# Kernel tuning notes

Measured on AMD Instinct MI355X. Metric: run time of the kernel, lower is better.

The kernel has to match this reference:

```python
import jax, jax.numpy as jnp
import numpy as np

_SAMPLING_EPS = 1e-5
NEG_INF = jnp.float32(-jnp.inf)


def setup_inputs() -> dict:
    key = jax.random.key(0)
    k1, k2, k3, k4, k5 = jax.random.split(key, 5)
    B, V = 128, 128000
    logits = jax.random.normal(k1, (B, V), dtype=jnp.float32) * 4.0
    # every 8th row is greedy (temperature 0), rest random in [0.1, 1.5)
    rand_t = 0.1 + 1.4 * jax.random.uniform(k2, (B,), dtype=jnp.float32)
    temperatures = jnp.where(jnp.arange(B) % 8 == 0, 0.0, rand_t)
    top_k = jax.random.randint(k3, (B,), 1, 1001, dtype=jnp.int64)
    top_p = 0.1 + 0.9 * jax.random.uniform(k4, (B,), dtype=jnp.float32)
    # q ~ Exponential(1), replaces torch's generator-based q.exponential_()
    exp_noise = jax.random.exponential(k5, (B, V), dtype=jnp.float32)
    return {"logits": logits, "temperatures": temperatures, "top_k": top_k,
            "top_p": top_p, "exp_noise": exp_noise}


def _masked_logits(logits, temperatures, top_k, top_p):
    B, V = logits.shape
    # apply_temperature: greedy rows (temp < eps) divide by 1.0
    temp = jnp.where(temperatures < _SAMPLING_EPS, 1.0, temperatures)
    x = logits / temp[:, None]                       # [B, V]
    # ascending sort (as in torch code)
    sort_idx = jnp.argsort(x, axis=-1)               # [B, V]
    x_sort = jnp.take_along_axis(x, sort_idx, axis=-1)
    # top-k: keep the k largest (last k of ascending sort)
    k = jnp.clip(top_k, None, V).astype(jnp.int32)
    thr_idx = (V - k)[:, None]                       # [B, 1]
    thr = jnp.take_along_axis(x_sort, thr_idx, axis=-1)
    x_sort = jnp.where(x_sort < thr, NEG_INF, x_sort)
    # top-p on the sorted (ascending) logits
    probs_sort = jax.nn.softmax(x_sort, axis=-1)
    probs_sum = jnp.cumsum(probs_sort, axis=-1)
    p_mask = probs_sum <= (1.0 - top_p)[:, None]
    p_mask = p_mask.at[:, -1].set(False)             # always keep the max
    x_sort = jnp.where(p_mask, NEG_INF, x_sort)
    # scatter back to original positions: out[b, sort_idx[b, j]] = x_sort[b, j]
    rows = jnp.arange(B)[:, None]
    return x.at[rows, sort_idx].set(x_sort)


def reference(logits, temperatures, top_k, top_p, exp_noise):
    logits = logits.astype(jnp.float32)
    greedy = jnp.argmax(logits, axis=-1)             # [B]
    masked = _masked_logits(logits, temperatures, top_k, top_p)
    probs = jax.nn.softmax(masked, axis=-1)
    # Gumbel-max / exponential-race sampling: argmax(probs / q)
    random_sampled = jnp.argmax(probs / exp_noise, axis=-1)
    sampled = jnp.where(temperatures < _SAMPLING_EPS, greedy, random_sampled)
    return sampled[:, None].astype(jnp.int32)        # SamplerOutput.sampled_token_ids
```

## Files before the change

kernel.cpp:

```cpp
#include <hip/hip_runtime.h>
#include <stdint.h>

#define CAP 4096
#define SL 20
#define THR1 256
#define THR4 1024
#define SEPS 1e-5f
#define ZMAX 8
#define LBUF 1024
#define KTHRF 8.0f
#define NB 4096
#define NBSH 13

typedef unsigned long long ull;

__device__ __forceinline__ uint32_t f2key(float x) {
  uint32_t u = __float_as_uint(x);
  return u ^ ((u & 0x80000000u) ? 0xFFFFFFFFu : 0x80000000u);
}
__device__ __forceinline__ float key2f(uint32_t k) {
  uint32_t u = (k & 0x80000000u) ? (k ^ 0x80000000u) : ~k;
  return __uint_as_float(u);
}

__global__ void k1_cap(const float* __restrict__ logits, const float* __restrict__ noise,
                       const float* __restrict__ temps,
                       ull* __restrict__ cand, unsigned int* __restrict__ cnt,
                       ull* __restrict__ rowmax, unsigned int* __restrict__ zcnt,
                       int* __restrict__ zlist, int B, int V, int slice_len) {
  __shared__ ull s_buf[LBUF];
  __shared__ unsigned int s_n, s_base;
  __shared__ ull s_w64[THR1 / 64];
  int tid = threadIdx.x;
  int lane = tid & 63, wid = tid >> 6;
  int half = B * SL;
  int bid = blockIdx.x;
  bool noise_side = bid >= half;
  if (noise_side) bid -= half;
  int row = bid / SL;
  int slice = bid % SL;
  float tr = temps[row];
  int col_base = slice * slice_len;
  int n4 = slice_len >> 2;
  int pairs = n4 >> 1;

  if (noise_side) {
    if (tr < SEPS) return;
    const float4* q4 = reinterpret_cast<const float4*>(noise + (size_t)row * V + col_base);
    for (int p = tid; p < pairs; p += THR1) {
      int v = p << 1;
      float4 q0 = q4[v];
      float4 q1 = q4[v + 1];
      float qs[8] = {q0.x, q0.y, q0.z, q0.w, q1.x, q1.y, q1.z, q1.w};
      bool anyz = (qs[0] == 0.f) | (qs[1] == 0.f) | (qs[2] == 0.f) | (qs[3] == 0.f) |
                  (qs[4] == 0.f) | (qs[5] == 0.f) | (qs[6] == 0.f) | (qs[7] == 0.f);
      if (anyz) {
        int c0 = col_base + 8 * p;
#pragma unroll
        for (int m = 0; m < 8; ++m) {
          if (qs[m] == 0.0f) {
            unsigned int zp = atomicAdd(&zcnt[row], 1u);
            if (zp < ZMAX) zlist[row * ZMAX + zp] = c0 + m;
          }
        }
      }
    }
    return;
  }

  const float4* p4 = reinterpret_cast<const float4*>(logits + (size_t)row * V + col_base);
  if (tr < SEPS) {
    ull best = 0ULL;
    for (int p = tid; p < pairs; p += THR1) {
      int v = p << 1;
      float4 f0 = p4[v];
      float4 f1 = p4[v + 1];
      int c0 = col_base + 8 * p;
      float xs[8] = {f0.x, f0.y, f0.z, f0.w, f1.x, f1.y, f1.z, f1.w};
#pragma unroll
      for (int m = 0; m < 8; ++m) {
        ull pk = ((ull)f2key(xs[m]) << 32) | (ull)(uint32_t)(V - 1 - (c0 + m));
        if (pk > best) best = pk;
      }
    }
    for (int off = 32; off > 0; off >>= 1) {
      ull o = __shfl_down(best, off);
      if (o > best) best = o;
    }
    if (lane == 0) s_w64[wid] = best;
    __syncthreads();
    if (tid == 0) {
      ull b2 = s_w64[0];
      for (int w = 1; w < THR1 / 64; ++w) if (s_w64[w] > b2) b2 = s_w64[w];
      atomicMax(&rowmax[row], b2);
    }
    return;
  }

  if (tid == 0) s_n = 0;
  __syncthreads();
  for (int p0 = 0; p0 < pairs; p0 += THR1) {
    int p = p0 + tid;
    unsigned int cm = 0;
    float fs[8];
    if (p < pairs) {
      int v = p << 1;
      float4 f0 = p4[v];
      float4 f1 = p4[v + 1];
      fs[0] = f0.x; fs[1] = f0.y; fs[2] = f0.z; fs[3] = f0.w;
      fs[4] = f1.x; fs[5] = f1.y; fs[6] = f1.z; fs[7] = f1.w;
#pragma unroll
      for (int m = 0; m < 8; ++m) cm |= (fs[m] >= KTHRF) ? (1u << m) : 0u;
    }
    unsigned int c8 = (unsigned int)__popc(cm);
    unsigned int inc = c8;
    for (int off = 1; off < 64; off <<= 1) {
      unsigned int o = __shfl_up(inc, off);
      if (lane >= off) inc += o;
    }
    unsigned int total = __shfl(inc, 63);
    if (total) {
      unsigned int base = 0;
      if (lane == 0) base = atomicAdd(&s_n, total);
      base = __shfl(base, 0);
      unsigned int off0 = base + inc - c8;
      if (cm) {
        int c0 = col_base + 8 * p;
#pragma unroll
        for (int m = 0; m < 8; ++m) {
          if (cm & (1u << m)) {
            uint32_t key = __float_as_uint(fs[m]) ^ 0x80000000u;
            ull pk = ((ull)key << 32) | (ull)(uint32_t)(c0 + m);
            if (off0 < LBUF) s_buf[off0] = pk;
            else {
              unsigned int g = atomicAdd(&cnt[row], 1u);
              if (g < CAP) cand[(size_t)row * CAP + g] = pk;
            }
            off0++;
          }
        }
      }
    }
  }
  __syncthreads();
  unsigned int m = (s_n < LBUF) ? s_n : LBUF;
  if (tid == 0) s_base = atomicAdd(&cnt[row], m);
  __syncthreads();
  unsigned int base = s_base;
  for (unsigned int i = tid; i < m; i += THR1) {
    unsigned int g = base + i;
    if (g < CAP) cand[(size_t)row * CAP + g] = s_buf[i];
  }
}

__global__ __launch_bounds__(THR4) void k4_final(
    const ull* __restrict__ cand, const unsigned int* __restrict__ cnt,
    const int* __restrict__ topk32, const float* __restrict__ temps,
    const float* __restrict__ topp, const float* __restrict__ noise,
    const ull* __restrict__ rowmax, const unsigned int* __restrict__ zcnt,
    const int* __restrict__ zlist, int* __restrict__ out, int B, int V) {
  __shared__ ull s_cand[CAP];
  __shared__ float s_e[CAP];
  __shared__ float s_q[CAP];
  __shared__ unsigned char s_kept[CAP];
  __shared__ float s_w[16];
  __shared__ unsigned int s_u[16];
  __shared__ ull s_w64[16];
  __shared__ int s_nan, s_pz, s_flag, s_pbin, s_m;
  int tid = threadIdx.x, row = blockIdx.x;
  int lane = tid & 63, wid = tid >> 6;
  float tr = temps[row];
  if (tr < SEPS) {
    if (tid == 0) {
      ull rm = rowmax[row];
      out[row] = V - 1 - (int)(uint32_t)(rm & 0xFFFFFFFFu);
    }
    return;
  }
  if (tid == 0) { s_nan = 0x7FFFFFFF; s_flag = 0; }
  unsigned int* hist = (unsigned int*)s_e;
  for (int b = tid; b < NB; b += THR4) hist[b] = 0;
  __syncthreads();
  if (tid < B && topk32[tid] == 0) s_flag = 1;

  unsigned int cv = cnt[row];
  int n = (cv < (unsigned int)CAP) ? (int)cv : CAP;
  if (n < 1) n = 1;
  uint32_t Kb = f2key(KTHRF / tr);
  ull held[4]; int nh = 0;
  for (int i = tid; i < n; i += THR4) {
    ull c = cand[(size_t)row * CAP + i];
    float x = key2f((uint32_t)(c >> 32)) / tr;
    uint32_t xk = f2key(x);
    held[nh++] = ((ull)xk << 32) | (c & 0xFFFFFFFFu);
    uint32_t bin = (xk - Kb) >> NBSH;
    if (bin > NB - 1) bin = NB - 1;
    atomicAdd(&hist[bin], 1u);
  }
  __syncthreads();
  int kraw = s_flag ? topk32[2 * row] : topk32[row];
  int kk = kraw < 1 ? 1 : (kraw > V ? V : kraw);
  if (kk > n) kk = n;
  unsigned int hb[4], csum = 0;
#pragma unroll
  for (int c = 0; c < 4; ++c) { hb[c] = hist[(tid << 2) + c]; csum += hb[c]; }
  unsigned int sfx = csum;
  for (int off = 1; off < 64; off <<= 1) {
    unsigned int o = __shfl_down(sfx, off);
    if (lane + off < 64) sfx += o;
  }
  if (lane == 0) s_u[wid] = sfx;
  __syncthreads();
  unsigned int above = sfx - csum;
  for (int w = wid + 1; w < 16; ++w) above += s_u[w];
  unsigned int run0 = above;
  for (int c = 3; c >= 0; --c) {
    unsigned int prev = run0;
    run0 += hb[c];
    if (run0 >= (unsigned int)kk && prev < (unsigned int)kk) {
      s_pbin = (tid << 2) + c;
      s_m = (int)run0;
    }
  }
  __syncthreads();
  uint32_t Pk = Kb + ((uint32_t)s_pbin << NBSH);
  int m = s_m;
  int myc = 0;
#pragma unroll
  for (int j = 0; j < 4; ++j)
    if (j < nh && (uint32_t)(held[j] >> 32) >= Pk) myc++;
  unsigned int inc = (unsigned int)myc;
  for (int off = 1; off < 64; off <<= 1) {
    unsigned int o = __shfl_up(inc, off);
    if (lane >= off) inc += o;
  }
  if (lane == 63) s_u[wid] = inc;
  __syncthreads();
  unsigned int base = inc - (unsigned int)myc;
  for (int w = 0; w < wid; ++w) base += s_u[w];
  int wpos = 0;
#pragma unroll
  for (int j = 0; j < 4; ++j)
    if (j < nh && (uint32_t)(held[j] >> 32) >= Pk) s_cand[base + (wpos++)] = held[j];
  int N = 64;
  while (N < m) N <<= 1;
  __syncthreads();
  for (int i = m + tid; i < N; i += THR4) s_cand[i] = 0ULL;
  __syncthreads();
  for (int k = 2; k <= 64; k <<= 1) {
    for (int j = k >> 1; j > 0; j >>= 1) {
      for (int i = tid; i < N; i += THR4) {
        int l = i ^ j;
        if (l > i) {
          ull a = s_cand[i], b = s_cand[l];
          bool up = ((i & k) == 0);
          if (up ? (a < b) : (a > b)) { s_cand[i] = b; s_cand[l] = a; }
        }
      }
      __builtin_amdgcn_wave_barrier();
    }
  }
  __syncthreads();
  for (int k = 128; k <= N; k <<= 1) {
    for (int j = k >> 1; j >= 64; j >>= 1) {
      for (int i = tid; i < N; i += THR4) {
        int l = i ^ j;
        if (l > i) {
          ull a = s_cand[i], b = s_cand[l];
          bool up = ((i & k) == 0);
          if (up ? (a < b) : (a > b)) { s_cand[i] = b; s_cand[l] = a; }
        }
      }
      __syncthreads();
    }
    for (int j = 32; j > 0; j >>= 1) {
      for (int i = tid; i < N; i += THR4) {
        int l = i ^ j;
        if (l > i) {
          ull a = s_cand[i], b = s_cand[l];
          bool up = ((i & k) == 0);
          if (up ? (a < b) : (a > b)) { s_cand[i] = b; s_cand[l] = a; }
        }
      }
      __builtin_amdgcn_wave_barrier();
    }
    __syncthreads();
  }
  uint32_t thrkey = (uint32_t)(s_cand[kk - 1] >> 32);
  float xmax = key2f((uint32_t)(s_cand[0] >> 32));
  int C = N / THR4;
  if (C < 1) C = 1;
  int i0 = tid * C;
  const float* qrow = noise + (size_t)row * V;
  float csumf = 0.f;
  for (int c = 0; c < C; ++c) {
    int i = i0 + c;
    if (i < N) {
      ull cd = s_cand[i];
      uint32_t key = (uint32_t)(cd >> 32);
      if (i < m) s_q[i] = qrow[(uint32_t)(cd & 0xFFFFFFFFu)];
      float e = 0.f;
      if (i < m && key >= thrkey) e = expf(key2f(key) - xmax);
      s_e[i] = e;
      csumf += e;
    }
  }
  {
    float v = csumf;
    for (int off = 32; off > 0; off >>= 1) v += __shfl_xor(v, off);
    if (lane == 0) s_w[wid] = v;
  }
  __syncthreads();
  float Z1 = 0.f;
  for (int w = 0; w < 16; ++w) Z1 += s_w[w];
  float pcsum = 0.f;
  for (int c = 0; c < C; ++c) {
    int i = i0 + c;
    if (i < N) pcsum += s_e[i] / Z1;
  }
  float sfx2 = pcsum;
  for (int off = 1; off < 64; off <<= 1) {
    float o = __shfl_down(sfx2, off);
    if (lane + off < 64) sfx2 += o;
  }
  __syncthreads();
  if (lane == 0) s_w[wid] = sfx2;
  __syncthreads();
  float abv = sfx2 - pcsum;
  for (int w = wid + 1; w < 16; ++w) abv += s_w[w];
  float thresh = 1.0f - topp[row];
  float run = abv, z2 = 0.f;
  for (int c = C - 1; c >= 0; --c) {
    int i = i0 + c;
    if (i < N) {
      run += s_e[i] / Z1;
      uint32_t key = (uint32_t)(s_cand[i] >> 32);
      bool kept = (i < m) && (key >= thrkey) && (run > thresh || i == 0);
      s_kept[i] = kept ? 1 : 0;
      if (kept) z2 += s_e[i];
    }
  }
  {
    float v = z2;
    for (int off = 32; off > 0; off >>= 1) v += __shfl_xor(v, off);
    __syncthreads();
    if (lane == 0) s_w[wid] = v;
  }
  __syncthreads();
  float Z2 = 0.f;
  for (int w = 0; w < 16; ++w) Z2 += s_w[w];
  unsigned int nzc = zcnt[row];
  int nz = (nzc < (unsigned int)ZMAX) ? (int)nzc : ZMAX;
  for (int zi = 0; zi < nz; ++zi) {
    int z = zlist[row * ZMAX + zi];
    if (tid == 0) s_pz = 0;
    __syncthreads();
    for (int c = 0; c < C; ++c) {
      int i = i0 + c;
      if (i < m && (int)(uint32_t)(s_cand[i] & 0xFFFFFFFFu) == z && s_kept[i] && s_e[i] > 0.f)
        s_pz = 1;
    }
    __syncthreads();
    if (tid == 0 && s_pz == 0 && z < s_nan) s_nan = z;
    __syncthreads();
  }
  ull pk = 0ULL;
  for (int c = 0; c < C; ++c) {
    int i = i0 + c;
    if (i < N && s_kept[i]) {
      int idx = (int)(uint32_t)(s_cand[i] & 0xFFFFFFFFu);
      float r = (s_e[i] / Z2) / s_q[i];
      ull p = ((ull)__float_as_uint(r) << 32) |
              (ull)(0xFFFFFFFFu - (uint32_t)idx);
      if (p > pk) pk = p;
    }
  }
  for (int off = 32; off > 0; off >>= 1) {
    ull o = __shfl_xor(pk, off);
    if (o > pk) pk = o;
  }
  if (lane == 0) s_w64[wid] = pk;
  __syncthreads();
  if (tid == 0) {
    ull best = s_w64[0];
    for (int w = 1; w < 16; ++w) if (s_w64[w] > best) best = s_w64[w];
    int winner = (int)(0xFFFFFFFFu - (uint32_t)(best & 0xFFFFFFFFu));
    if (s_nan != 0x7FFFFFFF) winner = s_nan;
    out[row] = winner;
  }
}

extern "C" void kernel_launch(void* const* d_in, const int* in_sizes, int n_in,
                              void* d_out, int out_size, void* d_ws, size_t ws_size,
                              hipStream_t stream) {
  const float* logits = (const float*)d_in[0];
  const float* temps  = (const float*)d_in[1];
  const int*   topk   = (const int*)d_in[2];
  const float* topp   = (const float*)d_in[3];
  const float* noise  = (const float*)d_in[4];
  int B = in_sizes[1];
  int V = in_sizes[0] / B;
  int slice = V / SL;

  char* ws = (char*)d_ws;
  size_t off = 0;
  ull* cand = (ull*)(ws + off); off += (size_t)B * CAP * 8;
  size_t zstart = off;
  ull* rowmax = (ull*)(ws + off); off += (size_t)B * 8;
  unsigned int* cnt = (unsigned int*)(ws + off); off += (size_t)B * 4;
  unsigned int* zcnt = (unsigned int*)(ws + off); off += (size_t)B * 4;
  size_t zend = off;
  int* zlist = (int*)(ws + off); off += (size_t)B * ZMAX * 4;

  hipMemsetAsync(ws + zstart, 0, zend - zstart, stream);
  k1_cap<<<dim3(2 * B * SL), dim3(THR1), 0, stream>>>(logits, noise, temps, cand, cnt,
                                                      rowmax, zcnt, zlist, B, V, slice);
  k4_final<<<dim3(B), dim3(THR4), 0, stream>>>(cand, cnt, topk, temps, topp, noise,
                                               rowmax, zcnt, zlist, (int*)d_out, B, V);
}
```

Before: 173.3 us.

## Widen per-thread loads to 16 floats and compact candidates per wavefront via ballot

Each thread in the candidate-capture kernel now loads four float4s (16 values) instead of two. The number of slices per row drops from 20 to 8, so fewer but larger blocks run. Candidate compaction changes from a shared atomic counter plus a shuffle prefix scan to per-wavefront ballot/mbcnt ranking into private 256-entry shared segments, which removes the shared-memory atomic and the scan. This trades more register pressure and longer per-block work for fewer instructions per element, and overflow past each wave's segment now falls back to global atomics sooner.

Measured after the change: 174.2 us, median of 2. Within noise of the previous version (+0.5%).

```diff
diff --git a/kernel.cpp b/kernel.cpp
--- a/kernel.cpp
+++ b/kernel.cpp
@@ -2,12 +2,12 @@
 #include <stdint.h>
 
 #define CAP 4096
-#define SL 20
+#define SL 8
 #define THR1 256
 #define THR4 1024
 #define SEPS 1e-5f
 #define ZMAX 8
-#define LBUF 1024
+#define WSEG 256
 #define KTHRF 8.0f
 #define NB 4096
 #define NBSH 13
@@ -23,13 +23,15 @@
   return __uint_as_float(u);
 }
 
-__global__ void k1_cap(const float* __restrict__ logits, const float* __restrict__ noise,
-                       const float* __restrict__ temps,
-                       ull* __restrict__ cand, unsigned int* __restrict__ cnt,
-                       ull* __restrict__ rowmax, unsigned int* __restrict__ zcnt,
-                       int* __restrict__ zlist, int B, int V, int slice_len) {
-  __shared__ ull s_buf[LBUF];
-  __shared__ unsigned int s_n, s_base;
+__global__ __launch_bounds__(THR1, 8) void k1_cap(
+    const float* __restrict__ logits, const float* __restrict__ noise,
+    const float* __restrict__ temps,
+    ull* __restrict__ cand, unsigned int* __restrict__ cnt,
+    ull* __restrict__ rowmax, unsigned int* __restrict__ zcnt,
+    int* __restrict__ zlist, int B, int V, int slice_len) {
+  __shared__ ull s_buf[4 * WSEG];
+  __shared__ unsigned int s_wn[4];
+  __shared__ unsigned int s_base;
   __shared__ ull s_w64[THR1 / 64];
   int tid = threadIdx.x;
   int lane = tid & 63, wid = tid >> 6;
@@ -41,23 +43,24 @@
   int slice = bid % SL;
   float tr = temps[row];
   int col_base = slice * slice_len;
-  int n4 = slice_len >> 2;
-  int pairs = n4 >> 1;
+  int groups = slice_len >> 4;
 
   if (noise_side) {
     if (tr < SEPS) return;
     const float4* q4 = reinterpret_cast<const float4*>(noise + (size_t)row * V + col_base);
-    for (int p = tid; p < pairs; p += THR1) {
-      int v = p << 1;
-      float4 q0 = q4[v];
-      float4 q1 = q4[v + 1];
-      float qs[8] = {q0.x, q0.y, q0.z, q0.w, q1.x, q1.y, q1.z, q1.w};
-      bool anyz = (qs[0] == 0.f) | (qs[1] == 0.f) | (qs[2] == 0.f) | (qs[3] == 0.f) |
-                  (qs[4] == 0.f) | (qs[5] == 0.f) | (qs[6] == 0.f) | (qs[7] == 0.f);
-      if (anyz) {
-        int c0 = col_base + 8 * p;
-#pragma unroll
-        for (int m = 0; m < 8; ++m) {
+    for (int g = tid; g < groups; g += THR1) {
+      const float4* p = q4 + (g << 2);
+      float4 a = p[0], b = p[1], c = p[2], d = p[3];
+      float m0 = fminf(fminf(fminf(a.x, a.y), fminf(a.z, a.w)),
+                       fminf(fminf(b.x, b.y), fminf(b.z, b.w)));
+      float m1 = fminf(fminf(fminf(c.x, c.y), fminf(c.z, c.w)),
+                       fminf(fminf(d.x, d.y), fminf(d.z, d.w)));
+      if (fminf(m0, m1) == 0.0f) {
+        float qs[16] = {a.x, a.y, a.z, a.w, b.x, b.y, b.z, b.w,
+                        c.x, c.y, c.z, c.w, d.x, d.y, d.z, d.w};
+        int c0 = col_base + (g << 4);
+#pragma unroll
+        for (int m = 0; m < 16; ++m) {
           if (qs[m] == 0.0f) {
             unsigned int zp = atomicAdd(&zcnt[row], 1u);
             if (zp < ZMAX) zlist[row * ZMAX + zp] = c0 + m;
@@ -71,14 +74,14 @@
   const float4* p4 = reinterpret_cast<const float4*>(logits + (size_t)row * V + col_base);
   if (tr < SEPS) {
     ull best = 0ULL;
-    for (int p = tid; p < pairs; p += THR1) {
-      int v = p << 1;
-      float4 f0 = p4[v];
-      float4 f1 = p4[v + 1];
-      int c0 = col_base + 8 * p;
-      float xs[8] = {f0.x, f0.y, f0.z, f0.w, f1.x, f1.y, f1.z, f1.w};
-#pragma unroll
-      for (int m = 0; m < 8; ++m) {
+    for (int g = tid; g < groups; g += THR1) {
+      const float4* p = p4 + (g << 2);
+      float4 a = p[0], b = p[1], c = p[2], d = p[3];
+      float xs[16] = {a.x, a.y, a.z, a.w, b.x, b.y, b.z, b.w,
+                      c.x, c.y, c.z, c.w, d.x, d.y, d.z, d.w};
+      int c0 = col_base + (g << 4);
+#pragma unroll
+      for (int m = 0; m < 16; ++m) {
         ull pk = ((ull)f2key(xs[m]) << 32) | (ull)(uint32_t)(V - 1 - (c0 + m));
         if (pk > best) best = pk;
       }
@@ -97,59 +100,58 @@
     return;
   }
 
-  if (tid == 0) s_n = 0;
-  __syncthreads();
-  for (int p0 = 0; p0 < pairs; p0 += THR1) {
-    int p = p0 + tid;
+  unsigned int wbase = 0;
+  for (int g0 = 0; g0 < groups; g0 += THR1) {
+    int g = g0 + tid;
     unsigned int cm = 0;
-    float fs[8];
-    if (p < pairs) {
-      int v = p << 1;
-      float4 f0 = p4[v];
-      float4 f1 = p4[v + 1];
-      fs[0] = f0.x; fs[1] = f0.y; fs[2] = f0.z; fs[3] = f0.w;
-      fs[4] = f1.x; fs[5] = f1.y; fs[6] = f1.z; fs[7] = f1.w;
-#pragma unroll
-      for (int m = 0; m < 8; ++m) cm |= (fs[m] >= KTHRF) ? (1u << m) : 0u;
-    }
-    unsigned int c8 = (unsigned int)__popc(cm);
-    unsigned int inc = c8;
-    for (int off = 1; off < 64; off <<= 1) {
-      unsigned int o = __shfl_up(inc, off);
-      if (lane >= off) inc += o;
-    }
-    unsigned int total = __shfl(inc, 63);
-    if (total) {
-      unsigned int base = 0;
-      if (lane == 0) base = atomicAdd(&s_n, total);
-      base = __shfl(base, 0);
-      unsigned int off0 = base + inc - c8;
-      if (cm) {
-        int c0 = col_base + 8 * p;
-#pragma unroll
-        for (int m = 0; m < 8; ++m) {
-          if (cm & (1u << m)) {
-            uint32_t key = __float_as_uint(fs[m]) ^ 0x80000000u;
-            ull pk = ((ull)key << 32) | (ull)(uint32_t)(c0 + m);
-            if (off0 < LBUF) s_buf[off0] = pk;
-            else {
-              unsigned int g = atomicAdd(&cnt[row], 1u);
-              if (g < CAP) cand[(size_t)row * CAP + g] = pk;
-            }
-            off0++;
-          }
+    float fs[16];
+    if (g < groups) {
+      const float4* p = p4 + (g << 2);
+      float4 a = p[0], b = p[1], c = p[2], d = p[3];
+      fs[0] = a.x; fs[1] = a.y; fs[2] = a.z; fs[3] = a.w;
+      fs[4] = b.x; fs[5] = b.y; fs[6] = b.z; fs[7] = b.w;
+      fs[8] = c.x; fs[9] = c.y; fs[10] = c.z; fs[11] = c.w;
+      fs[12] = d.x; fs[13] = d.y; fs[14] = d.z; fs[15] = d.w;
+#pragma unroll
+      for (int m = 0; m < 16; ++m) cm |= (fs[m] >= KTHRF) ? (1u << m) : 0u;
+    }
+    int c0 = col_base + (g << 4);
+    unsigned int run = 0;
+#pragma unroll
+    for (int m = 0; m < 16; ++m) {
+      ull bal = __ballot((cm >> m) & 1u);
+      if (cm & (1u << m)) {
+        unsigned int rk = __builtin_amdgcn_mbcnt_hi(
+            (uint32_t)(bal >> 32), __builtin_amdgcn_mbcnt_lo((uint32_t)bal, 0u));
+        unsigned int pos = wbase + run + rk;
+        uint32_t key = __float_as_uint(fs[m]) ^ 0x80000000u;
+        ull pk = ((ull)key << 32) | (ull)(uint32_t)(c0 + m);
+        if (pos < WSEG) s_buf[(wid << 8) + pos] = pk;
+        else {
+          unsigned int gg = atomicAdd(&cnt[row], 1u);
+          if (gg < CAP) cand[(size_t)row * CAP + gg] = pk;
         }
       }
-    }
-  }
-  __syncthreads();
-  unsigned int m = (s_n < LBUF) ? s_n : LBUF;
-  if (tid == 0) s_base = atomicAdd(&cnt[row], m);
-  __syncthreads();
-  unsigned int base = s_base;
-  for (unsigned int i = tid; i < m; i += THR1) {
-    unsigned int g = base + i;
-    if (g < CAP) cand[(size_t)row * CAP + g] = s_buf[i];
+      run += (unsigned int)__popcll(bal);
+    }
+    wbase += run;
+  }
+  if (lane == 0) s_wn[wid] = (wbase < WSEG) ? wbase : WSEG;
+  __syncthreads();
+  if (tid == 0) {
+    unsigned int t = s_wn[0] + s_wn[1] + s_wn[2] + s_wn[3];
+    s_base = atomicAdd(&cnt[row], t);
+  }
+  __syncthreads();
+  unsigned int b0 = s_base;
+  unsigned int doff = 0;
+  for (int w = 0; w < 4; ++w) {
+    unsigned int nw = s_wn[w];
+    for (unsigned int i = tid; i < nw; i += THR1) {
+      unsigned int gg = b0 + doff + i;
+      if (gg < CAP) cand[(size_t)row * CAP + gg] = s_buf[(w << 8) + i];
+    }
+    doff += nw;
   }
 }
 
```
